# Kernel tuning notes

Hardware: AMD Instinct MI355X
Metric: run time of the kernel (lower is better)

The kernel has to match this reference:

```python
import jax, jax.numpy as jnp
import numpy as np

B, H, T, D = 4, 8, 1024, 64
DECAY = 0.95


def setup_inputs() -> dict:
    key = jax.random.key(0)
    kq, kk, kv = jax.random.split(key, 3)
    q = jax.random.normal(kq, (B, H, T, D), dtype=jnp.float32)
    k = jax.random.normal(kk, (B, H, T, D), dtype=jnp.float32)
    v = jax.random.normal(kv, (B, H, T, D), dtype=jnp.float32)
    return {"q": q, "k": k, "v": v}


def reference(q, k, v):
    """Recurrent KV (linear-attention) scan.

    State: S_t = decay * S_{t-1} + k_t outer v_t  (per batch/head, [D, D])
    Out:   o_t = q_t @ S_t                         ([D])
    """
    decay = jnp.float32(DECAY)

    def step(S, qkv_t):
        q_t, k_t, v_t = qkv_t  # each [B, H, D]
        S = decay * S + jnp.einsum('bhd,bhe->bhde', k_t, v_t)  # [B,H,D,D]
        o_t = jnp.einsum('bhd,bhde->bhe', q_t, S)              # [B,H,D]
        return S, o_t

    S0 = jnp.zeros((B, H, D, D), dtype=q.dtype)
    # time-major for scan: [T, B, H, D]
    qT = jnp.moveaxis(q, 2, 0)
    kT = jnp.moveaxis(k, 2, 0)
    vT = jnp.moveaxis(v, 2, 0)
    _, oT = jax.lax.scan(step, S0, (qT, kT, vT))
    return jnp.moveaxis(oT, 0, 2)  # [B, H, T, D]
```

## Files before the change

kernel.cpp:

```cpp
#include <hip/hip_runtime.h>
#include <hip/hip_bf16.h>

#define D_    64
#define BH    32
#define LCH   64
#define NC    16
#define DECAY 0.95f
#define LN_D  0.051293294f
#define DEC64 0.03752432f
#define LDSB  68

typedef __attribute__((ext_vector_type(8))) short          bf8_t;
typedef __attribute__((ext_vector_type(8))) unsigned short u16x8;
typedef __attribute__((ext_vector_type(4))) float          f32x4;
typedef unsigned short u16;

static __device__ __forceinline__ u16 f2bf(float f) {
    return __builtin_bit_cast(u16, __float2bfloat16(f));
}
static __device__ __forceinline__ bf8_t frag_rr(float4 a, float4 b, float sc) {
    u16x8 r;
    r[0] = f2bf(a.x * sc); r[1] = f2bf(a.y * sc); r[2] = f2bf(a.z * sc); r[3] = f2bf(a.w * sc);
    r[4] = f2bf(b.x * sc); r[5] = f2bf(b.y * sc); r[6] = f2bf(b.z * sc); r[7] = f2bf(b.w * sc);
    return __builtin_bit_cast(bf8_t, r);
}
static __device__ __forceinline__ void stage_kv(const float4* kk, const float4* vv, float ksc,
                                                u16 (*KTb)[LDSB], u16 (*VTb)[LDSB],
                                                int sj, int sc0) {
    #pragma unroll
    for (int m = 0; m < 4; ++m) {
        const int cb = sc0 + 4 * m;
        KTb[cb + 0][sj] = f2bf(kk[m].x * ksc);
        KTb[cb + 1][sj] = f2bf(kk[m].y * ksc);
        KTb[cb + 2][sj] = f2bf(kk[m].z * ksc);
        KTb[cb + 3][sj] = f2bf(kk[m].w * ksc);
        VTb[cb + 0][sj] = f2bf(vv[m].x);
        VTb[cb + 1][sj] = f2bf(vv[m].y);
        VTb[cb + 2][sj] = f2bf(vv[m].z);
        VTb[cb + 3][sj] = f2bf(vv[m].w);
    }
}

__global__ __launch_bounds__(256, 3) void kv_fused(const float* __restrict__ q,
                                                   const float* __restrict__ k,
                                                   const float* __restrict__ v,
                                                   float* __restrict__ o) {
    __shared__ u16 KT[2][D_][LDSB];
    __shared__ u16 VT[2][D_][LDSB];
    u16 (*As)[LDSB] = KT[1];

    const int bid = (int)blockIdx.x;
    const int lb  = (bid & 7) * ((BH * NC) / 8) + (bid >> 3);
    const int bh  = lb >> 4;
    const int c   = lb & (NC - 1);

    const int tid  = threadIdx.x;
    const size_t bhb  = (size_t)bh * (NC * LCH) * D_;
    const size_t base = bhb + (size_t)c * LCH * D_;

    const int lane = tid & 63, w = tid >> 6;
    const int fr   = lane & 15, hi = lane >> 4;
    const int fk   = hi << 3;
    const int i0   = w << 4;
    const int ib   = i0 + (hi << 2);

    const int sj   = tid >> 2;
    const int sc0  = (tid & 3) << 4;

    const float* qrow = q + base + (size_t)(i0 + fr) * D_;
    const float4 qa0 = *(const float4*)(qrow + fk);
    const float4 qa1 = *(const float4*)(qrow + fk + 4);
    const float4 qb0 = *(const float4*)(qrow + 32 + fk);
    const float4 qb1 = *(const float4*)(qrow + 32 + fk + 4);
    float4 vo[4];
    {
        const float* vg = v + base + sj * D_ + sc0;
        #pragma unroll
        for (int m = 0; m < 4; ++m) vo[m] = *(const float4*)(vg + 4 * m);
    }

    float4 k1[4], v1[4], k0[4], v0[4];
    if (c >= 1) {
        const float* kg = k + base - (size_t)LCH * D_ + sj * D_ + sc0;
        const float* vg = v + base - (size_t)LCH * D_ + sj * D_ + sc0;
        #pragma unroll
        for (int m = 0; m < 4; ++m) { k1[m] = *(const float4*)(kg + 4*m);
                                      v1[m] = *(const float4*)(vg + 4*m); }
    }
    if (c >= 2) {
        const float* kg = k + base - (size_t)(2 * LCH) * D_ + sj * D_ + sc0;
        const float* vg = v + base - (size_t)(2 * LCH) * D_ + sj * D_ + sc0;
        #pragma unroll
        for (int m = 0; m < 4; ++m) { k0[m] = *(const float4*)(kg + 4*m);
                                      v0[m] = *(const float4*)(vg + 4*m); }
    }
    const float wdec = __expf(-LN_D * (float)(63 - sj));
    if (c >= 1) stage_kv(k1, v1, wdec,         KT[1], VT[1], sj, sc0);
    if (c >= 2) stage_kv(k0, v0, wdec * DEC64, KT[0], VT[0], sj, sc0);
    __syncthreads();

    f32x4 accS[4];
    #pragma unroll
    for (int m = 0; m < 4; ++m) accS[m] = (f32x4){0.f, 0.f, 0.f, 0.f};
    #pragma unroll
    for (int b = 1; b >= 0; --b) {
        if (c >= (2 - b)) {
            #pragma unroll
            for (int kt = 0; kt < 2; ++kt) {
                bf8_t av = *(const bf8_t*)&VT[b][i0 + fr][kt * 32 + fk];
                #pragma unroll
                for (int dt = 0; dt < 4; ++dt) {
                    bf8_t bk = *(const bf8_t*)&KT[b][dt * 16 + fr][kt * 32 + fk];
                    accS[dt] = __builtin_amdgcn_mfma_f32_16x16x32_bf16(av, bk, accS[dt], 0, 0, 0);
                }
            }
        }
    }
    __syncthreads();

    float4 kp[4][4];
    #pragma unroll
    for (int jt = 0; jt < 4; ++jt) {
        if (jt <= w) {
            const float* krow = k + base + (size_t)(jt * 16 + fr) * D_;
            kp[jt][0] = *(const float4*)(krow + fk);
            kp[jt][1] = *(const float4*)(krow + fk + 4);
            kp[jt][2] = *(const float4*)(krow + 32 + fk);
            kp[jt][3] = *(const float4*)(krow + 32 + fk + 4);
        }
    }

    if (c > 0) {
        #pragma unroll
        for (int dt = 0; dt < 4; ++dt)
            #pragma unroll
            for (int r = 0; r < 4; ++r)
                KT[0][ib + r][dt * 16 + fr] = f2bf(accS[dt][r]);
    }
    #pragma unroll
    for (int m = 0; m < 4; ++m) {
        const int cb = sc0 + 4 * m;
        VT[0][cb + 0][sj] = f2bf(vo[m].x);
        VT[0][cb + 1][sj] = f2bf(vo[m].y);
        VT[0][cb + 2][sj] = f2bf(vo[m].z);
        VT[0][cb + 3][sj] = f2bf(vo[m].w);
    }

    const bf8_t aq0 = frag_rr(qa0, qa1, 1.f);
    const bf8_t aq1 = frag_rr(qb0, qb1, 1.f);
    f32x4 accA[4];
    #pragma unroll
    for (int m = 0; m < 4; ++m) accA[m] = (f32x4){0.f, 0.f, 0.f, 0.f};
    #pragma unroll
    for (int jt = 0; jt < 4; ++jt) {
        if (jt <= w) {
            const float ksc = __expf(LN_D * (float)(jt * 16 + fr));
            bf8_t b0 = frag_rr(kp[jt][0], kp[jt][1], ksc);
            bf8_t b1 = frag_rr(kp[jt][2], kp[jt][3], ksc);
            accA[jt] = __builtin_amdgcn_mfma_f32_16x16x32_bf16(aq0, b0, accA[jt], 0, 0, 0);
            accA[jt] = __builtin_amdgcn_mfma_f32_16x16x32_bf16(aq1, b1, accA[jt], 0, 0, 0);
        }
    }

    const float db = __expf(-LN_D * (float)ib);
    float isc[4];
    isc[0] = db; isc[1] = db * DECAY; isc[2] = isc[1] * DECAY; isc[3] = isc[2] * DECAY;

    #pragma unroll
    for (int jt = 0; jt < 4; ++jt)
        #pragma unroll
        for (int r = 0; r < 4; ++r) {
            const int i  = ib + r;
            const int jj = jt * 16 + fr;
            float val = (jj <= i) ? accA[jt][r] * isc[r] : 0.f;
            As[i][jj] = f2bf(val);
        }
    __syncthreads();

    f32x4 accO[4];
    #pragma unroll
    for (int m = 0; m < 4; ++m) accO[m] = (f32x4){0.f, 0.f, 0.f, 0.f};
    if (c > 0) {
        #pragma unroll
        for (int et = 0; et < 4; ++et) {
            bf8_t b0 = *(const bf8_t*)&KT[0][et * 16 + fr][fk];
            bf8_t b1 = *(const bf8_t*)&KT[0][et * 16 + fr][32 + fk];
            accO[et] = __builtin_amdgcn_mfma_f32_16x16x32_bf16(aq0, b0, accO[et], 0, 0, 0);
            accO[et] = __builtin_amdgcn_mfma_f32_16x16x32_bf16(aq1, b1, accO[et], 0, 0, 0);
        }
    }
    #pragma unroll
    for (int et = 0; et < 4; ++et)
        #pragma unroll
        for (int r = 0; r < 4; ++r)
            accO[et][r] *= isc[r] * DECAY;

    const int nk2 = (w + 2) >> 1;
    #pragma unroll
    for (int kt2 = 0; kt2 < 2; ++kt2) {
        if (kt2 < nk2) {
            bf8_t aa = *(const bf8_t*)&As[i0 + fr][kt2 * 32 + fk];
            #pragma unroll
            for (int et = 0; et < 4; ++et) {
                bf8_t bv = *(const bf8_t*)&VT[0][et * 16 + fr][kt2 * 32 + fk];
                accO[et] = __builtin_amdgcn_mfma_f32_16x16x32_bf16(aa, bv, accO[et], 0, 0, 0);
            }
        }
    }

    float* og = o + base;
    #pragma unroll
    for (int et = 0; et < 4; ++et)
        #pragma unroll
        for (int r = 0; r < 4; ++r)
            og[(size_t)(ib + r) * D_ + et * 16 + fr] = accO[et][r];
}

extern "C" void kernel_launch(void* const* d_in, const int* in_sizes, int n_in,
                              void* d_out, int out_size, void* d_ws, size_t ws_size,
                              hipStream_t stream) {
    const float* q = (const float*)d_in[0];
    const float* k = (const float*)d_in[1];
    const float* v = (const float*)d_in[2];
    kv_fused<<<BH * NC, 256, 0, stream>>>(q, k, v, (float*)d_out);
}
```

Baseline: 14.86 us.

## Load previous-chunk V fragments directly from global and XOR-swizzle LDS transposes

Previous-chunk V tiles are now gathered straight from global memory into MFMA A-fragments with strided scalar loads, so they no longer pass through LDS, and the second VT buffer is removed. Transposed writes of K, V and the state tile into LDS use an XOR swizzle on the column index to cut bank conflicts, and the matching reads apply the same swizzle. The current-chunk V load and its LDS staging are moved later so they overlap with the intra-chunk QK compute. The cost is many uncoalesced 4-byte global loads for V, plus extra registers that may hurt occupancy.

```diff
diff --git a/kernel.cpp b/kernel.cpp
--- a/kernel.cpp
+++ b/kernel.cpp
@@ -24,21 +24,11 @@
     r[4] = f2bf(b.x * sc); r[5] = f2bf(b.y * sc); r[6] = f2bf(b.z * sc); r[7] = f2bf(b.w * sc);
     return __builtin_bit_cast(bf8_t, r);
 }
-static __device__ __forceinline__ void stage_kv(const float4* kk, const float4* vv, float ksc,
-                                                u16 (*KTb)[LDSB], u16 (*VTb)[LDSB],
-                                                int sj, int sc0) {
-    #pragma unroll
-    for (int m = 0; m < 4; ++m) {
-        const int cb = sc0 + 4 * m;
-        KTb[cb + 0][sj] = f2bf(kk[m].x * ksc);
-        KTb[cb + 1][sj] = f2bf(kk[m].y * ksc);
-        KTb[cb + 2][sj] = f2bf(kk[m].z * ksc);
-        KTb[cb + 3][sj] = f2bf(kk[m].w * ksc);
-        VTb[cb + 0][sj] = f2bf(vv[m].x);
-        VTb[cb + 1][sj] = f2bf(vv[m].y);
-        VTb[cb + 2][sj] = f2bf(vv[m].z);
-        VTb[cb + 3][sj] = f2bf(vv[m].w);
-    }
+static __device__ __forceinline__ bf8_t frag_g(const float* g) {
+    u16x8 r;
+    #pragma unroll
+    for (int z = 0; z < 8; ++z) r[z] = f2bf(g[z]);
+    return __builtin_bit_cast(bf8_t, r);
 }
 
 __global__ __launch_bounds__(256, 3) void kv_fused(const float* __restrict__ q,
@@ -46,7 +36,7 @@
                                                    const float* __restrict__ v,
                                                    float* __restrict__ o) {
     __shared__ u16 KT[2][D_][LDSB];
-    __shared__ u16 VT[2][D_][LDSB];
+    __shared__ u16 VT[D_][LDSB];
     u16 (*As)[LDSB] = KT[1];
 
     const int bid = (int)blockIdx.x;
@@ -66,55 +56,92 @@
 
     const int sj   = tid >> 2;
     const int sc0  = (tid & 3) << 4;
+    const int sjx  = sj ^ ((tid & 3) << 4);
+
+    float pv1[2][8], pv0[2][8];
+    if (c >= 1) {
+        const float* vs = v + base - (size_t)LCH * D_ + i0 + fr;
+        #pragma unroll
+        for (int kt = 0; kt < 2; ++kt)
+            #pragma unroll
+            for (int z = 0; z < 8; ++z)
+                pv1[kt][z] = vs[(size_t)(kt * 32 + fk + z) * D_];
+    }
+    if (c >= 2) {
+        const float* vs = v + base - (size_t)(2 * LCH) * D_ + i0 + fr;
+        #pragma unroll
+        for (int kt = 0; kt < 2; ++kt)
+            #pragma unroll
+            for (int z = 0; z < 8; ++z)
+                pv0[kt][z] = vs[(size_t)(kt * 32 + fk + z) * D_];
+    }
 
     const float* qrow = q + base + (size_t)(i0 + fr) * D_;
     const float4 qa0 = *(const float4*)(qrow + fk);
     const float4 qa1 = *(const float4*)(qrow + fk + 4);
     const float4 qb0 = *(const float4*)(qrow + 32 + fk);
     const float4 qb1 = *(const float4*)(qrow + 32 + fk + 4);
-    float4 vo[4];
-    {
-        const float* vg = v + base + sj * D_ + sc0;
-        #pragma unroll
-        for (int m = 0; m < 4; ++m) vo[m] = *(const float4*)(vg + 4 * m);
-    }
-
-    float4 k1[4], v1[4], k0[4], v0[4];
+
+    float4 k1[4], k0[4];
     if (c >= 1) {
         const float* kg = k + base - (size_t)LCH * D_ + sj * D_ + sc0;
-        const float* vg = v + base - (size_t)LCH * D_ + sj * D_ + sc0;
-        #pragma unroll
-        for (int m = 0; m < 4; ++m) { k1[m] = *(const float4*)(kg + 4*m);
-                                      v1[m] = *(const float4*)(vg + 4*m); }
+        #pragma unroll
+        for (int m = 0; m < 4; ++m) k1[m] = *(const float4*)(kg + 4 * m);
     }
     if (c >= 2) {
         const float* kg = k + base - (size_t)(2 * LCH) * D_ + sj * D_ + sc0;
-        const float* vg = v + base - (size_t)(2 * LCH) * D_ + sj * D_ + sc0;
-        #pragma unroll
-        for (int m = 0; m < 4; ++m) { k0[m] = *(const float4*)(kg + 4*m);
-                                      v0[m] = *(const float4*)(vg + 4*m); }
-    }
+        #pragma unroll
+        for (int m = 0; m < 4; ++m) k0[m] = *(const float4*)(kg + 4 * m);
+    }
+
     const float wdec = __expf(-LN_D * (float)(63 - sj));
-    if (c >= 1) stage_kv(k1, v1, wdec,         KT[1], VT[1], sj, sc0);
-    if (c >= 2) stage_kv(k0, v0, wdec * DEC64, KT[0], VT[0], sj, sc0);
+    if (c >= 1) {
+        #pragma unroll
+        for (int m = 0; m < 4; ++m) {
+            const int cb = sc0 + 4 * m;
+            KT[1][cb + 0][sjx] = f2bf(k1[m].x * wdec);
+            KT[1][cb + 1][sjx] = f2bf(k1[m].y * wdec);
+            KT[1][cb + 2][sjx] = f2bf(k1[m].z * wdec);
+            KT[1][cb + 3][sjx] = f2bf(k1[m].w * wdec);
+        }
+    }
+    if (c >= 2) {
+        const float wd0 = wdec * DEC64;
+        #pragma unroll
+        for (int m = 0; m < 4; ++m) {
+            const int cb = sc0 + 4 * m;
+            KT[0][cb + 0][sjx] = f2bf(k0[m].x * wd0);
+            KT[0][cb + 1][sjx] = f2bf(k0[m].y * wd0);
+            KT[0][cb + 2][sjx] = f2bf(k0[m].z * wd0);
+            KT[0][cb + 3][sjx] = f2bf(k0[m].w * wd0);
+        }
+    }
+
+    bf8_t av1[2], av0[2];
+    if (c >= 1) { av1[0] = frag_g(pv1[0]); av1[1] = frag_g(pv1[1]); }
+    if (c >= 2) { av0[0] = frag_g(pv0[0]); av0[1] = frag_g(pv0[1]); }
     __syncthreads();
 
     f32x4 accS[4];
     #pragma unroll
     for (int m = 0; m < 4; ++m) accS[m] = (f32x4){0.f, 0.f, 0.f, 0.f};
-    #pragma unroll
-    for (int b = 1; b >= 0; --b) {
-        if (c >= (2 - b)) {
-            #pragma unroll
-            for (int kt = 0; kt < 2; ++kt) {
-                bf8_t av = *(const bf8_t*)&VT[b][i0 + fr][kt * 32 + fk];
-                #pragma unroll
-                for (int dt = 0; dt < 4; ++dt) {
-                    bf8_t bk = *(const bf8_t*)&KT[b][dt * 16 + fr][kt * 32 + fk];
-                    accS[dt] = __builtin_amdgcn_mfma_f32_16x16x32_bf16(av, bk, accS[dt], 0, 0, 0);
-                }
+    if (c >= 1) {
+        #pragma unroll
+        for (int kt = 0; kt < 2; ++kt)
+            #pragma unroll
+            for (int dt = 0; dt < 4; ++dt) {
+                bf8_t bk = *(const bf8_t*)&KT[1][dt * 16 + fr][(kt * 32 + fk) ^ (dt << 4)];
+                accS[dt] = __builtin_amdgcn_mfma_f32_16x16x32_bf16(av1[kt], bk, accS[dt], 0, 0, 0);
             }
-        }
+    }
+    if (c >= 2) {
+        #pragma unroll
+        for (int kt = 0; kt < 2; ++kt)
+            #pragma unroll
+            for (int dt = 0; dt < 4; ++dt) {
+                bf8_t bk = *(const bf8_t*)&KT[0][dt * 16 + fr][(kt * 32 + fk) ^ (dt << 4)];
+                accS[dt] = __builtin_amdgcn_mfma_f32_16x16x32_bf16(av0[kt], bk, accS[dt], 0, 0, 0);
+            }
     }
     __syncthreads();
 
@@ -129,21 +156,19 @@
             kp[jt][3] = *(const float4*)(krow + 32 + fk + 4);
         }
     }
+    float4 vo[4];
+    {
+        const float* vg = v + base + sj * D_ + sc0;
+        #pragma unroll
+        for (int m = 0; m < 4; ++m) vo[m] = *(const float4*)(vg + 4 * m);
+    }
 
     if (c > 0) {
         #pragma unroll
         for (int dt = 0; dt < 4; ++dt)
             #pragma unroll
             for (int r = 0; r < 4; ++r)
-                KT[0][ib + r][dt * 16 + fr] = f2bf(accS[dt][r]);
-    }
-    #pragma unroll
-    for (int m = 0; m < 4; ++m) {
-        const int cb = sc0 + 4 * m;
-        VT[0][cb + 0][sj] = f2bf(vo[m].x);
-        VT[0][cb + 1][sj] = f2bf(vo[m].y);
-        VT[0][cb + 2][sj] = f2bf(vo[m].z);
-        VT[0][cb + 3][sj] = f2bf(vo[m].w);
+                KT[0][ib + r][((dt ^ w) << 4) + fr] = f2bf(accS[dt][r]);
     }
 
     const bf8_t aq0 = frag_rr(qa0, qa1, 1.f);
@@ -162,10 +187,17 @@
         }
     }
 
+    #pragma unroll
+    for (int m = 0; m < 4; ++m) {
+        const int cb = sc0 + 4 * m;
+        VT[cb + 0][sjx] = f2bf(vo[m].x);
+        VT[cb + 1][sjx] = f2bf(vo[m].y);
+        VT[cb + 2][sjx] = f2bf(vo[m].z);
+        VT[cb + 3][sjx] = f2bf(vo[m].w);
+    }
     const float db = __expf(-LN_D * (float)ib);
     float isc[4];
     isc[0] = db; isc[1] = db * DECAY; isc[2] = isc[1] * DECAY; isc[3] = isc[2] * DECAY;
-
     #pragma unroll
     for (int jt = 0; jt < 4; ++jt)
         #pragma unroll
@@ -183,8 +215,8 @@
     if (c > 0) {
         #pragma unroll
         for (int et = 0; et < 4; ++et) {
-            bf8_t b0 = *(const bf8_t*)&KT[0][et * 16 + fr][fk];
-            bf8_t b1 = *(const bf8_t*)&KT[0][et * 16 + fr][32 + fk];
+            bf8_t b0 = *(const bf8_t*)&KT[0][et * 16 + fr][(fk) ^ (et << 4)];
+            bf8_t b1 = *(const bf8_t*)&KT[0][et * 16 + fr][(32 + fk) ^ (et << 4)];
             accO[et] = __builtin_amdgcn_mfma_f32_16x16x32_bf16(aq0, b0, accO[et], 0, 0, 0);
             accO[et] = __builtin_amdgcn_mfma_f32_16x16x32_bf16(aq1, b1, accO[et], 0, 0, 0);
         }
@@ -202,7 +234,7 @@
             bf8_t aa = *(const bf8_t*)&As[i0 + fr][kt2 * 32 + fk];
             #pragma unroll
             for (int et = 0; et < 4; ++et) {
-                bf8_t bv = *(const bf8_t*)&VT[0][et * 16 + fr][kt2 * 32 + fk];
+                bf8_t bv = *(const bf8_t*)&VT[et * 16 + fr][(kt2 * 32 + fk) ^ (et << 4)];
                 accO[et] = __builtin_amdgcn_mfma_f32_16x16x32_bf16(aa, bv, accO[et], 0, 0, 0);
             }
         }
```

Result: faster. 14.23 us (-4.3%).
